# Kernel optimization log

Measured on AMD Instinct MI355X. Metric: run time of the kernel, lower is better.

Reference implementation:

```python
import jax, jax.numpy as jnp
import numpy as np

H, W, P = 480, 600, 2048
N = H * W
_IU = np.triu_indices(4)

def _conv(x, w, b, stride=1):
    y = jax.lax.conv_general_dilated(x, w, (stride, stride), 'SAME',
                                     dimension_numbers=('NCHW', 'OIHW', 'NCHW'))
    return y + b[None, :, None, None]

def _gn(x, scale, bias, groups=16, eps=1e-5):
    n, c, h, w = x.shape
    xg = x.reshape(n, groups, c // groups, h, w)
    mu = xg.mean(axis=(2, 3, 4), keepdims=True)
    var = xg.var(axis=(2, 3, 4), keepdims=True)
    xg = (xg - mu) * jax.lax.rsqrt(var + eps)
    return xg.reshape(n, c, h, w) * scale[None, :, None, None] + bias[None, :, None, None]

def _lrelu(x):
    return jnp.where(x >= 0, x, 0.2 * x)

def setup_inputs():
    key = jax.random.key(0)
    ks = jax.random.split(key, 16)
    def he(k, shape, fan_in):
        return jax.random.normal(k, shape, jnp.float32) * np.float32(np.sqrt(2.0 / fan_in))
    return {
        'depth': jax.random.normal(ks[0], (1, 1, H, W), jnp.float32),
        'pose': jax.random.normal(ks[1], (P, 2, 8), jnp.float32),
        'target_mask': (jax.random.uniform(ks[2], (1, 1, H, W)) > 0.5).astype(jnp.float32),
        'pairs': jax.random.randint(ks[3], (P, 2), 0, N),
        'conv1_w': he(ks[4], (32, 3, 3, 3), 3 * 9), 'conv1_b': jnp.zeros(32),
        'gn1_s': jnp.ones(32), 'gn1_b': jnp.zeros(32),
        'conv2_w': he(ks[5], (64, 32, 3, 3), 32 * 9), 'conv2_b': jnp.zeros(64),
        'gn2_s': jnp.ones(64), 'gn2_b': jnp.zeros(64),
        'conv3_w': he(ks[6], (64, 64, 3, 3), 64 * 9), 'conv3_b': jnp.zeros(64),
        'gn3_s': jnp.ones(64), 'gn3_b': jnp.zeros(64),
        'conv4_w': he(ks[7], (64, 96, 3, 3), 96 * 9), 'conv4_b': jnp.zeros(64),
        'gn4_s': jnp.ones(64), 'gn4_b': jnp.zeros(64),
        'gate_w': he(ks[8], (15, 64), 15), 'gate_b': jnp.zeros(64),
        'hid_w': he(ks[9], (64, 64), 64), 'hid_b': jnp.zeros(64),
        'out_w': he(ks[10], (64, 1), 64), 'out_b': jnp.zeros(1),
    }

def _forward(depth, pose, target_mask, params, pairs):
    (c1w, c1b, g1s, g1b, c2w, c2b, g2s, g2b, c3w, c3b, g3s, g3b,
     c4w, c4b, g4s, g4b, gw, gb, hw_, hb, ow, ob) = params
    idx = pairs[:, 0]
    hh, ww = idx // W, idx % W
    # vectorized replacement of the per-pair python-loop scatter
    attn = jnp.zeros((1, 1, H, W), jnp.float32).at[0, 0, hh, ww].set(1.0)
    std_depth = (depth - depth.mean()) * 10.0
    x = jnp.concatenate([std_depth, target_mask, attn], axis=1)  # [1,3,H,W]
    # res_unet backbone (encoder-decoder, GroupNorm, leaky-relu 0.2)
    c1 = _lrelu(_gn(_conv(x, c1w, c1b), g1s, g1b))               # [1,32,H,W]
    d1 = _lrelu(_gn(_conv(c1, c2w, c2b, stride=2), g2s, g2b))    # [1,64,H/2,W/2]
    bm = _lrelu(_gn(_conv(d1, c3w, c3b), g3s, g3b))              # [1,64,H/2,W/2]
    up = jax.image.resize(bm, (1, 64, H, W), method='nearest')
    u = jnp.concatenate([up, c1], axis=1)                         # [1,96,H,W]
    feats = _lrelu(_gn(_conv(u, c4w, c4b), g4s, g4b))            # [1,64,H,W]
    # vectorized per-pair gather
    fg = feats.reshape(64, N)[:, idx].T                           # [P,64]
    fg = jnp.broadcast_to(fg[:, None, :], (P, 2, 64))
    dg = std_depth.reshape(N)[idx]
    dg = jnp.broadcast_to(dg[:, None, None], (P, 2, 1))
    quat = pose[:, :, :4]
    fingers = pose[:, :, 4:7]
    trans = pose[:, :, 7:8]
    outer = quat[..., :, None] * quat[..., None, :]               # sign-invariant q_i*q_j
    enc = outer[..., _IU[0], _IU[1]]                              # [P,2,10]
    cond = jnp.concatenate([enc, fingers, trans, dg], axis=-1)    # [P,2,15]
    # ContextGate_1d: gated attention over gathered features
    gate = jax.nn.sigmoid(cond @ gw + gb)                         # [P,2,64]
    h = fg * gate
    h = h * jax.lax.rsqrt(jnp.sum(h * h, axis=-1, keepdims=True) + 1e-8)
    h = _lrelu(h @ hw_ + hb)
    return jax.nn.silu(h) @ ow + ob                               # [P,2,1]

def reference(depth, pose, target_mask, pairs, conv1_w, conv1_b, gn1_s, gn1_b,
              conv2_w, conv2_b, gn2_s, gn2_b, conv3_w, conv3_b, gn3_s, gn3_b,
              conv4_w, conv4_b, gn4_s, gn4_b, gate_w, gate_b, hid_w, hid_b,
              out_w, out_b):
    params = (conv1_w, conv1_b, gn1_s, gn1_b, conv2_w, conv2_b, gn2_s, gn2_b,
              conv3_w, conv3_b, gn3_s, gn3_b, conv4_w, conv4_b, gn4_s, gn4_b,
              gate_w, gate_b, hid_w, hid_b, out_w, out_b)
    return _forward(depth, pose, target_mask, params, pairs)
```

## Files before the change

kernel.cpp:

```cpp
#include <hip/hip_runtime.h>
#include <math.h>

#define HH 480
#define WW 600
#define NN (HH*WW)
#define PP 2048
#define H2 240
#define W2 300
#define N2 (H2*W2)

typedef __bf16  bf16x8  __attribute__((ext_vector_type(8)));
typedef float   f32x4   __attribute__((ext_vector_type(4)));
typedef ushort  ushort8 __attribute__((ext_vector_type(8)));

__device__ __forceinline__ ushort f2b(float f) {
    unsigned u = __float_as_uint(f);
    unsigned r = (u + 0x7FFF + ((u >> 16) & 1)) >> 16;
    return (ushort)r;
}
__device__ __forceinline__ float b2f(ushort u) {
    return __uint_as_float(((unsigned)u) << 16);
}

constexpr size_t alup(size_t x) { return (x + 4095) & ~(size_t)4095; }
constexpr size_t OFF_X    = 4096;
constexpr size_t OFF_C1R  = alup(OFF_X   + 3UL*NN*4);
constexpr size_t OFF_RW2  = alup(OFF_C1R + 32UL*NN*2);
constexpr size_t OFF_RW3  = alup(OFF_RW2 + 64UL*N2*2);
constexpr size_t OFF_WB2  = alup(OFF_RW3 + 64UL*N2*2);
constexpr size_t OFF_WB3  = alup(OFF_WB2 + 36864UL);
constexpr size_t OFF_WB4  = alup(OFF_WB3 + 73728UL);
constexpr size_t OFF_SLOT = alup(OFF_WB4 + 110592UL);
constexpr size_t OFF_CMP  = alup(OFF_SLOT + (size_t)NN*4);

__global__ void k_sum(const float* __restrict__ d, float* __restrict__ ws) {
    float s = 0.f;
    for (int i = blockIdx.x*blockDim.x + threadIdx.x; i < NN; i += gridDim.x*blockDim.x)
        s += d[i];
    #pragma unroll
    for (int o = 32; o; o >>= 1) s += __shfl_down(s, o, 64);
    __shared__ float sm[4];
    int wid = threadIdx.x >> 6;
    if ((threadIdx.x & 63) == 0) sm[wid] = s;
    __syncthreads();
    if (threadIdx.x == 0) {
        float t = 0.f;
        for (int w = 0; w < (int)(blockDim.x >> 6); ++w) t += sm[w];
        atomicAdd(ws, t);
    }
}

__global__ void k_buildx(const float* __restrict__ depth, const float* __restrict__ mask,
                         const float* __restrict__ ws, float* __restrict__ x) {
    int i = blockIdx.x*blockDim.x + threadIdx.x;
    if (i >= NN) return;
    float mean = ws[0] * (1.0f/NN);
    x[i]        = (depth[i] - mean) * 10.0f;
    x[NN + i]   = mask[i];
    x[2*NN + i] = 0.f;
}

__global__ void k_scatter(const int* __restrict__ pairs, float* __restrict__ x) {
    int p = blockIdx.x*blockDim.x + threadIdx.x;
    if (p < PP) x[2*NN + pairs[2*p]] = 1.0f;
}

__global__ void k_slot(const int* __restrict__ pairs, int* __restrict__ slotmap) {
    int p = blockIdx.x*blockDim.x + threadIdx.x;
    if (p < PP) slotmap[pairs[2*p]] = p;
}

__global__ void k_wcvt(const float* __restrict__ w, ushort* __restrict__ dst, int NCH) {
    int e = blockIdx.x*256 + threadIdx.x;
    int total = 9*NCH*64*32;
    if (e >= total) return;
    int k  = e & 31;
    int co = (e >> 5) & 63;
    int rest = e >> 11;
    int c = rest % NCH;
    int t = rest / NCH;
    dst[e] = f2b(w[(co*(NCH*32) + c*32 + k)*9 + t]);
}

template<int CIN, int TCO, int YPB>
__global__ __launch_bounds__(64) void k_conv1(const float* __restrict__ in,
        const float* __restrict__ w, const float* __restrict__ bias,
        ushort* __restrict__ outb, float* __restrict__ stat) {
    int x    = blockIdx.x*64 + threadIdx.x;
    int lane = threadIdx.x;
    int co0  = blockIdx.z*TCO;
    bool valid = x < WW;
    float s[TCO/2], s2[TCO/2];
    #pragma unroll
    for (int j = 0; j < TCO/2; ++j) { s[j] = 0.f; s2[j] = 0.f; }

    int  xb   = x - 1;
    bool xint = (xb >= 0) && (xb + 2 < WW);

    for (int yy = 0; yy < YPB; ++yy) {
        int y = blockIdx.y*YPB + yy;
        float acc[TCO];
        #pragma unroll
        for (int c = 0; c < TCO; ++c) acc[c] = bias[co0+c];
        for (int ci = 0; ci < CIN; ++ci) {
            const float* ip = in + (long)ci*NN;
            float iv[3][3];
            #pragma unroll
            for (int dy = 0; dy < 3; ++dy) {
                int iy = y + dy - 1;
                if ((unsigned)iy < (unsigned)HH) {
                    const float* rp = ip + (long)iy*WW + xb;
                    if (xint) { iv[dy][0]=rp[0]; iv[dy][1]=rp[1]; iv[dy][2]=rp[2]; }
                    else {
                        #pragma unroll
                        for (int dx = 0; dx < 3; ++dx) {
                            int ix = xb + dx;
                            iv[dy][dx] = ((unsigned)ix < (unsigned)WW) ? ip[(long)iy*WW+ix] : 0.f;
                        }
                    }
                } else iv[dy][0]=iv[dy][1]=iv[dy][2]=0.f;
            }
            const float* wp = w + ((long)co0*CIN + ci)*9;
            #pragma unroll
            for (int c = 0; c < TCO; ++c)
                #pragma unroll
                for (int k = 0; k < 9; ++k)
                    acc[c] += iv[k/3][k%3] * wp[(long)c*CIN*9 + k];
        }
        if (valid) {
            ushort8 p0, p1;
            #pragma unroll
            for (int j = 0; j < 8; ++j) { p0[j] = f2b(acc[j]); p1[j] = f2b(acc[8+j]); }
            ushort* op = outb + (size_t)(y*WW + x)*32 + co0;
            *(ushort8*)op     = p0;
            *(ushort8*)(op+8) = p1;
            #pragma unroll
            for (int j = 0; j < TCO/2; ++j) {
                float a = acc[2*j], b = acc[2*j+1];
                s[j]  += a + b;
                s2[j] += a*a + b*b;
            }
        }
    }

    #pragma unroll
    for (int o = 1; o < 64; o <<= 1)
        #pragma unroll
        for (int j = 0; j < TCO/2; ++j) {
            s[j]  += __shfl_xor(s[j],  o, 64);
            s2[j] += __shfl_xor(s2[j], o, 64);
        }
    float vs = 0.f, vq = 0.f;
    #pragma unroll
    for (int j = 0; j < TCO/2; ++j) {
        vs = (lane == j)            ? s[j]  : vs;
        vq = (lane == j + TCO/2)    ? s2[j] : vq;
    }
    if (lane < TCO) {
        int g0 = co0 >> 1;
        int addr = (lane < TCO/2) ? (g0 + lane) : (16 + g0 + lane - TCO/2);
        atomicAdd(&stat[addr], (lane < TCO/2) ? vs : vq);
    }
}

template<int MODE>
__global__ __launch_bounds__(256) void k_sconv(
        const ushort* __restrict__ inA, const ushort* __restrict__ inB,
        const ushort* __restrict__ wb, const float* __restrict__ bias,
        const float* __restrict__ gsA, const float* __restrict__ gbA, const float* __restrict__ stA,
        const float* __restrict__ gsB, const float* __restrict__ gbB, const float* __restrict__ stB,
        ushort* __restrict__ outb,
        const int* __restrict__ slotmap, float* __restrict__ compact,
        float* __restrict__ stat) {
    constexpr int Wo   = (MODE==4) ? WW : W2;
    constexpr int NCH  = (MODE==2) ? 1 : (MODE==3) ? 2 : 3;
    constexpr int NPT  = (MODE==2) ? 2 : 4;
    constexpr int ROWS = (MODE==2) ? 9 : 6;
    constexpr int PXS  = 68;
    constexpr int CPITCH = 36;
    constexpr int UNITS = ROWS*PXS*4;
    constexpr int Hi = (MODE==3) ? H2 : HH;
    constexpr int Wi = (MODE==3) ? W2 : WW;
    __shared__ __align__(16) ushort sh[ROWS*PXS*CPITCH];
    __shared__ float sred[4][16][2];

    int w    = threadIdx.x >> 6;
    int lane = threadIdx.x & 63;
    int lm   = lane & 15;
    int lg   = lane >> 4;
    int q    = threadIdx.x & 3;
    int y0   = blockIdx.y*4;
    int x0   = blockIdx.x*(NPT*16);
    int y    = y0 + w;
    int iy0  = (MODE==2) ? 2*y0 : y0 - 1;
    int ix0  = (MODE==2) ? 2*x0 : x0 - 1;

    f32x4 acc[4][NPT];
    #pragma unroll
    for (int ct = 0; ct < 4; ++ct)
        #pragma unroll
        for (int pt = 0; pt < NPT; ++pt) acc[ct][pt] = 0.f;

    int dsbase = (((MODE==2 ? 2*w*PXS + 2*lm : w*PXS + lm))*CPITCH + lg*8);

    #pragma unroll
    for (int kc = 0; kc < NCH; ++kc) {
        if (kc) __syncthreads();
        float Ac[8], Bc[8];
        {
            const bool useB = (MODE==4) && (kc == 2);
            const float* gs = useB ? gsB : gsA;
            const float* gb = useB ? gbB : gbA;
            const float* st = useB ? stB : stA;
            const float cnt = (MODE==2 || useB) ? 2.0f*(float)NN : 4.0f*(float)N2;
            const int   shp = (MODE==2 || useB) ? 1 : 2;
            const int   cb  = (MODE==2 || useB) ? q*8 : kc*32 + q*8;
            #pragma unroll
            for (int j = 0; j < 8; ++j) {
                int c = cb + j, g = c >> shp;
                float mu  = st[g] / cnt;
                float var = st[16+g] / cnt - mu*mu;
                float rs  = rsqrtf(var + 1e-5f);
                float a   = rs * gs[c];
                Ac[j] = a; Bc[j] = gb[c] - mu*a;
            }
        }
        #pragma unroll
        for (int u0 = 0; u0 < UNITS; u0 += 256) {
            int u = u0 + threadIdx.x;
            if (u < UNITS) {
                int r  = u / (PXS*4);
                int rm = u - r*(PXS*4);
                int px = rm >> 2;
                int iy = iy0 + r;
                int ix = ix0 + px;
                ushort8 pk = {};
                if ((unsigned)iy < (unsigned)Hi && (unsigned)ix < (unsigned)Wi) {
                    const ushort* sp;
                    if (MODE==2)      sp = inA + ((size_t)iy*WW + ix)*32 + q*8;
                    else if (MODE==3) sp = inA + ((size_t)iy*W2 + ix)*64 + kc*32 + q*8;
                    else if (kc < 2)  sp = inA + ((size_t)(iy>>1)*W2 + (ix>>1))*64 + kc*32 + q*8;
                    else              sp = inB + ((size_t)iy*WW + ix)*32 + q*8;
                    ushort8 raw = *(const ushort8*)sp;
                    #pragma unroll
                    for (int j = 0; j < 8; ++j) {
                        float t = b2f(raw[j])*Ac[j] + Bc[j];
                        pk[j] = f2b(t >= 0.f ? t : 0.2f*t);
                    }
                }
                *(ushort8*)&sh[(r*PXS + px)*CPITCH + q*8] = pk;
            }
        }
        __syncthreads();
        #pragma unroll
        for (int t = 0; t < 9; ++t) {
            const int dy = t/3, dx = t - 3*(t/3);
            const ushort* wp = wb + (size_t)((t*NCH + kc)*64)*32;
            bf16x8 a[4];
            #pragma unroll
            for (int ct = 0; ct < 4; ++ct)
                a[ct] = *(const bf16x8*)(wp + (ct*16 + lm)*32 + lg*8);
            #pragma unroll
            for (int pt = 0; pt < NPT; ++pt) {
                int off = (dy*PXS + (MODE==2 ? pt*32 + dx : pt*16 + dx))*CPITCH;
                bf16x8 b = *(const bf16x8*)&sh[dsbase + off];
                #pragma unroll
                for (int ct = 0; ct < 4; ++ct)
                    acc[ct][pt] = __builtin_amdgcn_mfma_f32_16x16x32_bf16(a[ct], b, acc[ct][pt], 0, 0, 0);
            }
        }
    }

    if (MODE != 4) {
        #pragma unroll
        for (int ct = 0; ct < 4; ++ct) {
            float s = 0.f, s2 = 0.f;
            #pragma unroll
            for (int pt = 0; pt < NPT; ++pt) {
                int pxg = x0 + pt*16 + lm;
                bool vld = pxg < Wo;
                ushort4 pk;
                #pragma unroll
                for (int reg = 0; reg < 4; ++reg) {
                    int co = ct*16 + lg*4 + reg;
                    float v = acc[ct][pt][reg] + bias[co];
                    ((ushort*)&pk)[reg] = f2b(v);
                    if (vld) { s += v; s2 += v*v; }
                }
                if (vld)
                    *(ushort4*)(outb + (size_t)(y*Wo + pxg)*64 + ct*16 + lg*4) = pk;
            }
            #pragma unroll
            for (int o = 1; o < 16; o <<= 1) {
                s  += __shfl_xor(s,  o, 64);
                s2 += __shfl_xor(s2, o, 64);
            }
            if (lm == 0) { sred[w][ct*4+lg][0] = s; sred[w][ct*4+lg][1] = s2; }
        }
    } else {
        int slots[4];
        #pragma unroll
        for (int pt = 0; pt < 4; ++pt) {
            int pxg = x0 + pt*16 + lm;
            slots[pt] = (pxg < Wo) ? slotmap[(size_t)y*Wo + pxg] : -1;
        }
        #pragma unroll
        for (int ct = 0; ct < 4; ++ct) {
            float s = 0.f, s2 = 0.f;
            #pragma unroll
            for (int pt = 0; pt < 4; ++pt) {
                int pxg = x0 + pt*16 + lm;
                bool vld = pxg < Wo;
                f32x4 r;
                #pragma unroll
                for (int reg = 0; reg < 4; ++reg) {
                    int co = ct*16 + lg*4 + reg;
                    float v = acc[ct][pt][reg] + bias[co];
                    r[reg] = v;
                    if (vld) { s += v; s2 += v*v; }
                }
                if (slots[pt] >= 0)
                    *(f32x4*)(compact + (size_t)slots[pt]*64 + ct*16 + lg*4) = r;
            }
            #pragma unroll
            for (int o = 1; o < 16; o <<= 1) {
                s  += __shfl_xor(s,  o, 64);
                s2 += __shfl_xor(s2, o, 64);
            }
            if (lm == 0) { sred[w][ct*4+lg][0] = s; sred[w][ct*4+lg][1] = s2; }
        }
    }
    __syncthreads();
    if (threadIdx.x < 32) {
        int g = threadIdx.x >> 1, k = threadIdx.x & 1;
        float t = sred[0][g][k] + sred[1][g][k] + sred[2][g][k] + sred[3][g][k];
        atomicAdd(&stat[k*16 + g], t);
    }
}

__global__ void k_mlp(const float* __restrict__ pose, const float* __restrict__ sd,
                      const int* __restrict__ pairs, const int* __restrict__ slotmap,
                      const float* __restrict__ compact,
                      const float* __restrict__ g4s, const float* __restrict__ g4b,
                      const float* __restrict__ st4,
                      const float* __restrict__ gw, const float* __restrict__ gb,
                      const float* __restrict__ hw, const float* __restrict__ hb,
                      const float* __restrict__ ow, const float* __restrict__ ob,
                      float* __restrict__ out) {
    int wid  = threadIdx.x >> 6;
    int lane = threadIdx.x & 63;
    int t = blockIdx.x*4 + wid;
    int p = t >> 1;
    const float* pp = pose + t*8;
    float q0=pp[0], q1=pp[1], q2=pp[2], q3=pp[3];
    float f0=pp[4], f1=pp[5], f2=pp[6], tr=pp[7];
    int idx = pairs[2*p];
    float dg = sd[idx];
    float cond[15] = {q0*q0,q0*q1,q0*q2,q0*q3,q1*q1,q1*q2,q1*q3,q2*q2,q2*q3,q3*q3,
                      f0,f1,f2,tr,dg};
    float acc = gb[lane];
    #pragma unroll
    for (int k = 0; k < 15; ++k) acc += cond[k]*gw[k*64+lane];
    float gate = 1.f/(1.f+expf(-acc));
    int slot = slotmap[idx];
    float raw = compact[(size_t)slot*64 + lane];
    int   g4  = lane >> 2;
    float cnt = 4.0f * (float)NN;
    float mu  = st4[g4] / cnt;
    float var = st4[16+g4] / cnt - mu*mu;
    float rs  = rsqrtf(var + 1e-5f);
    float fv  = (raw - mu) * rs * g4s[lane] + g4b[lane];
    float fg  = fv >= 0.f ? fv : 0.2f*fv;
    float h = fg*gate;
    float ss = h*h;
    #pragma unroll
    for (int o = 32; o; o >>= 1) ss += __shfl_xor(ss, o, 64);
    h *= rsqrtf(ss + 1e-8f);
    __shared__ float hs[4][64];
    hs[wid][lane] = h;
    __syncthreads();
    float a2 = hb[lane];
    #pragma unroll 8
    for (int d = 0; d < 64; ++d) a2 += hs[wid][d]*hw[d*64+lane];
    float h2 = a2 >= 0.f ? a2 : 0.2f*a2;
    float si = h2 / (1.f+expf(-h2));
    float v = si * ow[lane];
    #pragma unroll
    for (int o = 32; o; o >>= 1) v += __shfl_xor(v, o, 64);
    if (lane == 0) out[t] = v + ob[0];
}

extern "C" void kernel_launch(void* const* d_in, const int* in_sizes, int n_in,
                              void* d_out, int out_size, void* d_ws, size_t ws_size,
                              hipStream_t stream) {
    const float* depth = (const float*)d_in[0];
    const float* pose  = (const float*)d_in[1];
    const float* mask  = (const float*)d_in[2];
    const int*   pairs = (const int*)  d_in[3];
    const float* c1w = (const float*)d_in[4];  const float* c1b = (const float*)d_in[5];
    const float* g1s = (const float*)d_in[6];  const float* g1b = (const float*)d_in[7];
    const float* c2w = (const float*)d_in[8];  const float* c2b = (const float*)d_in[9];
    const float* g2s = (const float*)d_in[10]; const float* g2b = (const float*)d_in[11];
    const float* c3w = (const float*)d_in[12]; const float* c3b = (const float*)d_in[13];
    const float* g3s = (const float*)d_in[14]; const float* g3b = (const float*)d_in[15];
    const float* c4w = (const float*)d_in[16]; const float* c4b = (const float*)d_in[17];
    const float* g4s = (const float*)d_in[18]; const float* g4b = (const float*)d_in[19];
    const float* gw  = (const float*)d_in[20]; const float* gb  = (const float*)d_in[21];
    const float* hw_ = (const float*)d_in[22]; const float* hb  = (const float*)d_in[23];
    const float* ow  = (const float*)d_in[24]; const float* ob  = (const float*)d_in[25];

    char* base = (char*)d_ws;
    float*  stats = (float*) base;
    float*  X    = (float*) (base + OFF_X);
    ushort* C1R  = (ushort*)(base + OFF_C1R);
    ushort* RW2  = (ushort*)(base + OFF_RW2);
    ushort* RW3  = (ushort*)(base + OFF_RW3);
    ushort* WB2  = (ushort*)(base + OFF_WB2);
    ushort* WB3  = (ushort*)(base + OFF_WB3);
    ushort* WB4  = (ushort*)(base + OFF_WB4);
    int*    SLOT = (int*)   (base + OFF_SLOT);
    float*  CMP  = (float*) (base + OFF_CMP);
    float* st1 = stats + 16;
    float* st2 = stats + 64;
    float* st3 = stats + 112;
    float* st4 = stats + 160;

    hipMemsetAsync(d_ws, 0, 1024, stream);
    hipMemsetAsync(SLOT, 0xFF, (size_t)NN*4, stream);

    k_sum    <<<1024, 256, 0, stream>>>(depth, stats);
    k_buildx <<<(NN+255)/256, 256, 0, stream>>>(depth, mask, stats, X);
    k_scatter<<<(PP+255)/256, 256, 0, stream>>>(pairs, X);
    k_slot   <<<(PP+255)/256, 256, 0, stream>>>(pairs, SLOT);
    k_wcvt   <<< 72, 256, 0, stream>>>(c2w, WB2, 1);
    k_wcvt   <<<144, 256, 0, stream>>>(c3w, WB3, 2);
    k_wcvt   <<<216, 256, 0, stream>>>(c4w, WB4, 3);

    k_conv1<3,16,8><<<dim3(10, 60, 2), 64, 0, stream>>>(X, c1w, c1b, C1R, st1);

    k_sconv<2><<<dim3(10, 60), 256, 0, stream>>>(C1R, nullptr, WB2, c2b,
        g1s, g1b, st1, nullptr, nullptr, nullptr, RW2, nullptr, nullptr, st2);

    k_sconv<3><<<dim3(5, 60), 256, 0, stream>>>(RW2, nullptr, WB3, c3b,
        g2s, g2b, st2, nullptr, nullptr, nullptr, RW3, nullptr, nullptr, st3);

    k_sconv<4><<<dim3(10, 120), 256, 0, stream>>>(RW3, C1R, WB4, c4b,
        g3s, g3b, st3, g1s, g1b, st1, nullptr, SLOT, CMP, st4);

    k_mlp<<<(2*PP)/4, 256, 0, stream>>>(pose, X, pairs, SLOT, CMP, g4s, g4b, st4,
                                        gw, gb, hw_, hb, ow, ob, (float*)d_out);
}
```

Before: 384.2 us.

## Prefetch next channel chunk into registers during MFMA; use native bf16 converts

The sconv kernel now loads the next input channel chunk from global memory into registers before running the MFMA loop on the current chunk. This hides global load latency behind compute. The manual bit-twiddled float/bf16 conversions are replaced with native __bf16 casts, and fmaxf is used for the leaky ReLU. The cost is more live registers from the staging buffers, which may reduce occupancy.

```diff
diff --git a/kernel.cpp b/kernel.cpp
--- a/kernel.cpp
+++ b/kernel.cpp
@@ -10,6 +10,7 @@
 #define N2 (H2*W2)
 
 typedef __bf16  bf16x8  __attribute__((ext_vector_type(8)));
+typedef __bf16  bf16x4  __attribute__((ext_vector_type(4)));
 typedef float   f32x4   __attribute__((ext_vector_type(4)));
 typedef ushort  ushort8 __attribute__((ext_vector_type(8)));
 
@@ -17,9 +18,6 @@
     unsigned u = __float_as_uint(f);
     unsigned r = (u + 0x7FFF + ((u >> 16) & 1)) >> 16;
     return (ushort)r;
-}
-__device__ __forceinline__ float b2f(ushort u) {
-    return __uint_as_float(((unsigned)u) << 16);
 }
 
 constexpr size_t alup(size_t x) { return (x + 4095) & ~(size_t)4095; }
@@ -128,12 +126,12 @@
                     acc[c] += iv[k/3][k%3] * wp[(long)c*CIN*9 + k];
         }
         if (valid) {
-            ushort8 p0, p1;
-            #pragma unroll
-            for (int j = 0; j < 8; ++j) { p0[j] = f2b(acc[j]); p1[j] = f2b(acc[8+j]); }
+            bf16x8 p0, p1;
+            #pragma unroll
+            for (int j = 0; j < 8; ++j) { p0[j] = (__bf16)acc[j]; p1[j] = (__bf16)acc[8+j]; }
             ushort* op = outb + (size_t)(y*WW + x)*32 + co0;
-            *(ushort8*)op     = p0;
-            *(ushort8*)(op+8) = p1;
+            *(ushort8*)op     = __builtin_bit_cast(ushort8, p0);
+            *(ushort8*)(op+8) = __builtin_bit_cast(ushort8, p1);
             #pragma unroll
             for (int j = 0; j < TCO/2; ++j) {
                 float a = acc[2*j], b = acc[2*j+1];
@@ -153,8 +151,8 @@
     float vs = 0.f, vq = 0.f;
     #pragma unroll
     for (int j = 0; j < TCO/2; ++j) {
-        vs = (lane == j)            ? s[j]  : vs;
-        vq = (lane == j + TCO/2)    ? s2[j] : vq;
+        vs = (lane == j)         ? s[j]  : vs;
+        vq = (lane == j + TCO/2) ? s2[j] : vq;
     }
     if (lane < TCO) {
         int g0 = co0 >> 1;
@@ -179,6 +177,7 @@
     constexpr int PXS  = 68;
     constexpr int CPITCH = 36;
     constexpr int UNITS = ROWS*PXS*4;
+    constexpr int NLD  = (UNITS + 255)/256;
     constexpr int Hi = (MODE==3) ? H2 : HH;
     constexpr int Wi = (MODE==3) ? W2 : WW;
     __shared__ __align__(16) ushort sh[ROWS*PXS*CPITCH];
@@ -203,9 +202,39 @@
 
     int dsbase = (((MODE==2 ? 2*w*PXS + 2*lm : w*PXS + lm))*CPITCH + lg*8);
 
+    ushort8  stg[NLD];
+    unsigned vmask = 0;
+
+    auto LOADR = [&](int kc) {
+        vmask = 0;
+        #pragma unroll
+        for (int i = 0; i < NLD; ++i) {
+            int u = i*256 + (int)threadIdx.x;
+            ushort8 v = {};
+            if (u < UNITS) {
+                int r  = u / (PXS*4);
+                int rm = u - r*(PXS*4);
+                int px = rm >> 2;
+                int iy = iy0 + r;
+                int ix = ix0 + px;
+                if ((unsigned)iy < (unsigned)Hi && (unsigned)ix < (unsigned)Wi) {
+                    const ushort* sp;
+                    if (MODE==2)      sp = inA + ((size_t)iy*WW + ix)*32 + q*8;
+                    else if (MODE==3) sp = inA + ((size_t)iy*W2 + ix)*64 + kc*32 + q*8;
+                    else if (kc < 2)  sp = inA + ((size_t)(iy>>1)*W2 + (ix>>1))*64 + kc*32 + q*8;
+                    else              sp = inB + ((size_t)iy*WW + ix)*32 + q*8;
+                    v = *(const ushort8*)sp;
+                    vmask |= (1u << i);
+                }
+            }
+            stg[i] = v;
+        }
+    };
+
+    LOADR(0);
+
     #pragma unroll
     for (int kc = 0; kc < NCH; ++kc) {
-        if (kc) __syncthreads();
         float Ac[8], Bc[8];
         {
             const bool useB = (MODE==4) && (kc == 2);
@@ -225,33 +254,28 @@
                 Ac[j] = a; Bc[j] = gb[c] - mu*a;
             }
         }
-        #pragma unroll
-        for (int u0 = 0; u0 < UNITS; u0 += 256) {
-            int u = u0 + threadIdx.x;
+        if (kc) __syncthreads();
+        #pragma unroll
+        for (int i = 0; i < NLD; ++i) {
+            int u = i*256 + (int)threadIdx.x;
             if (u < UNITS) {
                 int r  = u / (PXS*4);
                 int rm = u - r*(PXS*4);
                 int px = rm >> 2;
-                int iy = iy0 + r;
-                int ix = ix0 + px;
-                ushort8 pk = {};
-                if ((unsigned)iy < (unsigned)Hi && (unsigned)ix < (unsigned)Wi) {
-                    const ushort* sp;
-                    if (MODE==2)      sp = inA + ((size_t)iy*WW + ix)*32 + q*8;
-                    else if (MODE==3) sp = inA + ((size_t)iy*W2 + ix)*64 + kc*32 + q*8;
-                    else if (kc < 2)  sp = inA + ((size_t)(iy>>1)*W2 + (ix>>1))*64 + kc*32 + q*8;
-                    else              sp = inB + ((size_t)iy*WW + ix)*32 + q*8;
-                    ushort8 raw = *(const ushort8*)sp;
-                    #pragma unroll
-                    for (int j = 0; j < 8; ++j) {
-                        float t = b2f(raw[j])*Ac[j] + Bc[j];
-                        pk[j] = f2b(t >= 0.f ? t : 0.2f*t);
-                    }
+                bf16x8 raw = __builtin_bit_cast(bf16x8, stg[i]);
+                bool val = (vmask >> i) & 1;
+                bf16x8 o;
+                #pragma unroll
+                for (int j = 0; j < 8; ++j) {
+                    float t = (float)raw[j]*Ac[j] + Bc[j];
+                    t = fmaxf(t, 0.2f*t);
+                    o[j] = (__bf16)(val ? t : 0.f);
                 }
-                *(ushort8*)&sh[(r*PXS + px)*CPITCH + q*8] = pk;
+                *(ushort8*)&sh[(r*PXS + px)*CPITCH + q*8] = __builtin_bit_cast(ushort8, o);
             }
         }
         __syncthreads();
+        if (kc + 1 < NCH) LOADR(kc + 1);
         #pragma unroll
         for (int t = 0; t < 9; ++t) {
             const int dy = t/3, dx = t - 3*(t/3);
@@ -279,16 +303,16 @@
             for (int pt = 0; pt < NPT; ++pt) {
                 int pxg = x0 + pt*16 + lm;
                 bool vld = pxg < Wo;
-                ushort4 pk;
+                bf16x4 pk;
                 #pragma unroll
                 for (int reg = 0; reg < 4; ++reg) {
                     int co = ct*16 + lg*4 + reg;
                     float v = acc[ct][pt][reg] + bias[co];
-                    ((ushort*)&pk)[reg] = f2b(v);
+                    pk[reg] = (__bf16)v;
                     if (vld) { s += v; s2 += v*v; }
                 }
                 if (vld)
-                    *(ushort4*)(outb + (size_t)(y*Wo + pxg)*64 + ct*16 + lg*4) = pk;
+                    *(bf16x4*)(outb + (size_t)(y*Wo + pxg)*64 + ct*16 + lg*4) = pk;
             }
             #pragma unroll
             for (int o = 1; o < 16; o <<= 1) {
```

New measurement: 317.0 us. 17.5% less time.
